# Optimization experiments

Measured on AMD Instinct MI355X. Metric: run time of the kernel, lower is better.

The kernel has to match this reference:

```python
import jax, jax.numpy as jnp
import numpy as np

N = 10000      # nodes (attention_adj_matrix_shape = (N, N))
E = 320000     # edges, avg degree 32
D_IN = 256     # input feature dim
D_H = 256      # hidden_units = [256]
ALPHA = 0.2    # leaky_relu slope for attention activation


def setup_inputs() -> dict:
    key = jax.random.key(0)
    k_x, k_src, k_dst, k_w1, k_b1, k_wa, k_ba = jax.random.split(key, 7)
    node_features = jax.random.normal(k_x, (N, D_IN), dtype=jnp.float32)
    # edges sorted by source column (tf.math.segment_sum requires sorted segment ids)
    src = jnp.sort(jax.random.randint(k_src, (E,), 0, N))
    dst = jax.random.randint(k_dst, (E,), 0, N)
    edges = jnp.stack([src, dst], axis=1).astype(jnp.int64)
    # hidden_layer: single Dense(256) (linear, keras Dense default activation=None)
    W1 = jax.random.normal(k_w1, (D_IN, D_H), dtype=jnp.float32) / np.sqrt(D_IN)
    b1 = jnp.zeros((D_H,), dtype=jnp.float32)
    # attention_layer: Dense(1) then activation
    Wa = jax.random.normal(k_wa, (2 * D_H, 1), dtype=jnp.float32) / np.sqrt(2 * D_H)
    ba = jnp.zeros((1,), dtype=jnp.float32)
    return {"node_features": node_features, "edges": edges,
            "W1": W1, "b1": b1, "Wa": Wa, "ba": ba}


def reference(node_features, edges, W1, b1, Wa, ba):
    n = node_features.shape[0]
    # hidden projection
    feats = node_features @ W1 + b1                       # [N, D_H]
    src, dst = edges[:, 0], edges[:, 1]
    # pairwise gather + concat: [E, 2*D_H]
    pair = jnp.concatenate([feats[src], feats[dst]], axis=1)
    scores = jax.nn.leaky_relu((pair @ Wa + ba)[:, 0], ALPHA)  # [E]
    # segment softmax over source node (matches exp / segment_sum / gather)
    ex = jnp.exp(scores)
    denom = jax.ops.segment_sum(ex, src, num_segments=n)       # [N]
    alpha = ex / denom[src]                                     # [E]
    # dense scatter of attention weights (scatter_nd sums duplicates)
    A = jnp.zeros((n, n), dtype=feats.dtype).at[src, dst].add(alpha)
    # add_self_features=False -> plain aggregate
    return A @ feats                                            # [N, D_H]
```

## Files before the change

kernel.cpp:

```cpp
#include <hip/hip_runtime.h>
#include <hip/hip_bf16.h>

#define N_NODES 10000
#define E_EDGES 320000
#define D 256
#define LRELU_ALPHA 0.2f


using short8  = __attribute__((ext_vector_type(8))) short;
using floatx4 = __attribute__((ext_vector_type(4))) float;
using bf16 = __hip_bfloat16;

__device__ __forceinline__ float bu2f(unsigned short u) {
    return __uint_as_float((unsigned)u << 16);
}
__device__ __forceinline__ unsigned short f2bu(float f) {
    union { bf16 b; unsigned short u; } cv;
    cv.b = __float2bfloat16(f);
    return cv.u;
}

__global__ __launch_bounds__(256) void prep(const int* __restrict__ raw,
                                            int* __restrict__ dst,
                                            int* __restrict__ row_start) {
    bool is64 = true;
    #pragma unroll
    for (int t = 0; t < 16; ++t)
        if (raw[2 * t + 1] != 0) is64 = false;

    int e = blockIdx.x * 256 + threadIdx.x;
    if (e >= E_EDGES) return;
    int s, d, sprev;
    if (is64) { s = raw[4 * e]; d = raw[4 * e + 2]; sprev = e ? raw[4 * e - 4] : -1; }
    else      { s = raw[2 * e]; d = raw[2 * e + 1]; sprev = e ? raw[2 * e - 2] : -1; }
    dst[e] = d;
    for (int r = sprev + 1; r <= s; ++r) row_start[r] = e;
    if (e == E_EDGES - 1)
        for (int r = s + 1; r <= N_NODES; ++r) row_start[r] = E_EDGES;
}

__global__ __launch_bounds__(256) void wprep(const float* __restrict__ W1,
                                             bf16* __restrict__ W1f) {
    const int id = blockIdx.x * 256 + threadIdx.x;
    const int j = id & 7, l = (id >> 3) & 63, t = (id >> 9) & 15, s = id >> 13;
    const int k = s * 32 + (l >> 4) * 8 + j;
    const int n = t * 16 + (l & 15);
    W1f[id] = __float2bfloat16(W1[k * D + n]);
}

__global__ __launch_bounds__(256) void gemm_mfma(const float* __restrict__ X,
                                                 const bf16* __restrict__ W1f,
                                                 const float* __restrict__ b1,
                                                 const float* __restrict__ Wa,
                                                 bf16* __restrict__ featsb,
                                                 float* __restrict__ a_src,
                                                 float* __restrict__ a_dst) {
    const int w = threadIdx.x >> 6, l = threadIdx.x & 63;
    const int quad = l >> 4, lan = l & 15;
    const int row0 = blockIdx.x * 16;

    floatx4 acc[4] = {{0.f, 0.f, 0.f, 0.f}, {0.f, 0.f, 0.f, 0.f},
                      {0.f, 0.f, 0.f, 0.f}, {0.f, 0.f, 0.f, 0.f}};

    const float4* Ax = (const float4*)(X + (size_t)(row0 + lan) * D);
    const short8* B8 = (const short8*)W1f;

    #pragma unroll
    for (int s = 0; s < 8; ++s) {
        const float4 u = Ax[s * 8 + quad * 2];
        const float4 v = Ax[s * 8 + quad * 2 + 1];
        short8 af;
        af[0] = (short)f2bu(u.x); af[1] = (short)f2bu(u.y);
        af[2] = (short)f2bu(u.z); af[3] = (short)f2bu(u.w);
        af[4] = (short)f2bu(v.x); af[5] = (short)f2bu(v.y);
        af[6] = (short)f2bu(v.z); af[7] = (short)f2bu(v.w);
        #pragma unroll
        for (int t = 0; t < 4; ++t) {
            const short8 bf = B8[(s * 16 + (4 * w + t)) * 64 + l];
            acc[t] = __builtin_amdgcn_mfma_f32_16x16x32_bf16(af, bf, acc[t], 0, 0, 0);
        }
    }

    float p1[4] = {0.f, 0.f, 0.f, 0.f}, p2[4] = {0.f, 0.f, 0.f, 0.f};
    #pragma unroll
    for (int t = 0; t < 4; ++t) {
        const int n = (4 * w + t) * 16 + lan;
        const float bias = b1[n], wa1 = Wa[n], wa2 = Wa[D + n];
        #pragma unroll
        for (int r = 0; r < 4; ++r) {
            const float v = acc[t][r] + bias;
            featsb[(size_t)(row0 + quad * 4 + r) * D + n] = __float2bfloat16(v);
            p1[r] += v * wa1;
            p2[r] += v * wa2;
        }
    }

    __shared__ float red1[4][16], red2[4][16];
    #pragma unroll
    for (int r = 0; r < 4; ++r) {
        #pragma unroll
        for (int off = 1; off < 16; off <<= 1) {
            p1[r] += __shfl_xor(p1[r], off);
            p2[r] += __shfl_xor(p2[r], off);
        }
        if (lan == 0) { red1[w][quad * 4 + r] = p1[r]; red2[w][quad * 4 + r] = p2[r]; }
    }
    __syncthreads();
    if (threadIdx.x < 16) {
        const int m = threadIdx.x;
        a_src[row0 + m] = red1[0][m] + red1[1][m] + red1[2][m] + red1[3][m];
        a_dst[row0 + m] = red2[0][m] + red2[1][m] + red2[2][m] + red2[3][m];
    }
}

__global__ __launch_bounds__(256) void aggregate_half(const int* __restrict__ dst,
                                                      const int* __restrict__ row_start,
                                                      const float* __restrict__ a_src,
                                                      const float* __restrict__ a_dst,
                                                      const float* __restrict__ ba,
                                                      const unsigned short* __restrict__ featsb,
                                                      float* __restrict__ out,
                                                      const int half) {
    const int i = blockIdx.x * 4 + (threadIdx.x >> 6);
    const int l = threadIdx.x & 63;
    const int rs = row_start[i], re = row_start[i + 1];
    const float base = a_src[i] + ba[0];
    const unsigned int* F = (const unsigned int*)featsb;
    const int off = half * 64 + l;

    float2 acc = {0.f, 0.f};
    float dsum = 0.f;

    int e = rs;
    for (; e + 8 <= re; e += 8) {
        unsigned int fw[8];
        float xv[8];
        #pragma unroll
        for (int u = 0; u < 8; ++u) {
            const int d = dst[e + u];
            fw[u] = F[(size_t)d * 128 + off];
            float s = base + a_dst[d];
            s = (s > 0.f) ? s : LRELU_ALPHA * s;
            xv[u] = expf(s);
        }
        #pragma unroll
        for (int u = 0; u < 8; ++u) {
            acc.x += xv[u] * bu2f((unsigned short)(fw[u] & 0xffff));
            acc.y += xv[u] * bu2f((unsigned short)(fw[u] >> 16));
            dsum += xv[u];
        }
    }
    for (; e < re; ++e) {
        const int d = dst[e];
        const unsigned int f = F[(size_t)d * 128 + off];
        float s = base + a_dst[d];
        s = (s > 0.f) ? s : LRELU_ALPHA * s;
        const float x = expf(s);
        acc.x += x * bu2f((unsigned short)(f & 0xffff));
        acc.y += x * bu2f((unsigned short)(f >> 16));
        dsum += x;
    }

    const float inv = (re > rs) ? 1.f / dsum : 0.f;
    float2 o;
    o.x = acc.x * inv;
    o.y = acc.y * inv;
    ((float2*)out)[(size_t)i * 128 + off] = o;
}

extern "C" void kernel_launch(void* const* d_in, const int* in_sizes, int n_in,
                              void* d_out, int out_size, void* d_ws, size_t ws_size,
                              hipStream_t stream) {
    const float* X     = (const float*)d_in[0];
    const int*   edges = (const int*)d_in[1];
    const float* W1    = (const float*)d_in[2];
    const float* b1    = (const float*)d_in[3];
    const float* Wa    = (const float*)d_in[4];
    const float* ba    = (const float*)d_in[5];
    float* out = (float*)d_out;

    bf16* featsb = (bf16*)d_ws;
    bf16* W1f    = featsb + (size_t)N_NODES * D;
    float* a_src = (float*)(W1f + 65536);
    float* a_dst = a_src + N_NODES;
    int*   dstv  = (int*)(a_dst + N_NODES);
    int*   row_start = dstv + E_EDGES;

    prep<<<(E_EDGES + 255) / 256, 256, 0, stream>>>(edges, dstv, row_start);
    wprep<<<65536 / 256, 256, 0, stream>>>(W1, W1f);
    gemm_mfma<<<N_NODES / 16, 256, 0, stream>>>(X, W1f, b1, Wa, featsb, a_src, a_dst);
    aggregate_half<<<N_NODES / 4, 256, 0, stream>>>(dstv, row_start, a_src, a_dst, ba,
                                                    (const unsigned short*)featsb, out, 0);
    aggregate_half<<<N_NODES / 4, 256, 0, stream>>>(dstv, row_start, a_src, a_dst, ba,
                                                    (const unsigned short*)featsb, out, 1);
}
```

Before: 123.0 us.

## Precompute per-edge attention weights in prep and merge aggregate halves into one pass

```diff
diff --git a/kernel.cpp b/kernel.cpp
--- a/kernel.cpp
+++ b/kernel.cpp
@@ -18,25 +18,6 @@
     union { bf16 b; unsigned short u; } cv;
     cv.b = __float2bfloat16(f);
     return cv.u;
-}
-
-__global__ __launch_bounds__(256) void prep(const int* __restrict__ raw,
-                                            int* __restrict__ dst,
-                                            int* __restrict__ row_start) {
-    bool is64 = true;
-    #pragma unroll
-    for (int t = 0; t < 16; ++t)
-        if (raw[2 * t + 1] != 0) is64 = false;
-
-    int e = blockIdx.x * 256 + threadIdx.x;
-    if (e >= E_EDGES) return;
-    int s, d, sprev;
-    if (is64) { s = raw[4 * e]; d = raw[4 * e + 2]; sprev = e ? raw[4 * e - 4] : -1; }
-    else      { s = raw[2 * e]; d = raw[2 * e + 1]; sprev = e ? raw[2 * e - 2] : -1; }
-    dst[e] = d;
-    for (int r = sprev + 1; r <= s; ++r) row_start[r] = e;
-    if (e == E_EDGES - 1)
-        for (int r = s + 1; r <= N_NODES; ++r) row_start[r] = E_EDGES;
 }
 
 __global__ __launch_bounds__(256) void wprep(const float* __restrict__ W1,
@@ -113,59 +94,71 @@
     }
 }
 
-__global__ __launch_bounds__(256) void aggregate_half(const int* __restrict__ dst,
-                                                      const int* __restrict__ row_start,
-                                                      const float* __restrict__ a_src,
-                                                      const float* __restrict__ a_dst,
-                                                      const float* __restrict__ ba,
-                                                      const unsigned short* __restrict__ featsb,
-                                                      float* __restrict__ out,
-                                                      const int half) {
+__global__ __launch_bounds__(256) void prep(const int* __restrict__ raw,
+                                            const float* __restrict__ a_src,
+                                            const float* __restrict__ a_dst,
+                                            const float* __restrict__ ba,
+                                            int2* __restrict__ edata,
+                                            int* __restrict__ row_start) {
+    bool is64 = true;
+    #pragma unroll
+    for (int t = 0; t < 16; ++t)
+        if (raw[2 * t + 1] != 0) is64 = false;
+
+    int e = blockIdx.x * 256 + threadIdx.x;
+    if (e >= E_EDGES) return;
+    int s, d, sprev;
+    if (is64) { s = raw[4 * e]; d = raw[4 * e + 2]; sprev = e ? raw[4 * e - 4] : -1; }
+    else      { s = raw[2 * e]; d = raw[2 * e + 1]; sprev = e ? raw[2 * e - 2] : -1; }
+
+    float sc = a_src[s] + a_dst[d] + ba[0];
+    sc = (sc > 0.f) ? sc : LRELU_ALPHA * sc;
+    edata[e] = make_int2(d, __float_as_int(expf(sc)));
+
+    for (int r = sprev + 1; r <= s; ++r) row_start[r] = e;
+    if (e == E_EDGES - 1)
+        for (int r = s + 1; r <= N_NODES; ++r) row_start[r] = E_EDGES;
+}
+
+__global__ __launch_bounds__(256) void aggregate(const int2* __restrict__ edata,
+                                                 const int* __restrict__ row_start,
+                                                 const unsigned short* __restrict__ featsb,
+                                                 float* __restrict__ out) {
     const int i = blockIdx.x * 4 + (threadIdx.x >> 6);
     const int l = threadIdx.x & 63;
     const int rs = row_start[i], re = row_start[i + 1];
-    const float base = a_src[i] + ba[0];
-    const unsigned int* F = (const unsigned int*)featsb;
-    const int off = half * 64 + l;
+    const ushort4* F = (const ushort4*)featsb;
 
-    float2 acc = {0.f, 0.f};
+    float4 acc = {0.f, 0.f, 0.f, 0.f};
     float dsum = 0.f;
 
     int e = rs;
     for (; e + 8 <= re; e += 8) {
-        unsigned int fw[8];
-        float xv[8];
+        int2 ed[8];
+        #pragma unroll
+        for (int u = 0; u < 8; ++u) ed[u] = edata[e + u];
         #pragma unroll
         for (int u = 0; u < 8; ++u) {
-            const int d = dst[e + u];
-            fw[u] = F[(size_t)d * 128 + off];
-            float s = base + a_dst[d];
-            s = (s > 0.f) ? s : LRELU_ALPHA * s;
-            xv[u] = expf(s);
-        }
-        #pragma unroll
-        for (int u = 0; u < 8; ++u) {
-            acc.x += xv[u] * bu2f((unsigned short)(fw[u] & 0xffff));
-            acc.y += xv[u] * bu2f((unsigned short)(fw[u] >> 16));
-            dsum += xv[u];
+            const ushort4 f = F[(size_t)ed[u].x * 64 + l];
+            const float x = __int_as_float(ed[u].y);
+            acc.x += x * bu2f(f.x); acc.y += x * bu2f(f.y);
+            acc.z += x * bu2f(f.z); acc.w += x * bu2f(f.w);
+            dsum += x;
         }
     }
     for (; e < re; ++e) {
-        const int d = dst[e];
-        const unsigned int f = F[(size_t)d * 128 + off];
-        float s = base + a_dst[d];
-        s = (s > 0.f) ? s : LRELU_ALPHA * s;
-        const float x = expf(s);
-        acc.x += x * bu2f((unsigned short)(f & 0xffff));
-        acc.y += x * bu2f((unsigned short)(f >> 16));
+        const int2 ed = edata[e];
+        const ushort4 f = F[(size_t)ed.x * 64 + l];
+        const float x = __int_as_float(ed.y);
+        acc.x += x * bu2f(f.x); acc.y += x * bu2f(f.y);
+        acc.z += x * bu2f(f.z); acc.w += x * bu2f(f.w);
         dsum += x;
     }
 
     const float inv = (re > rs) ? 1.f / dsum : 0.f;
-    float2 o;
-    o.x = acc.x * inv;
-    o.y = acc.y * inv;
-    ((float2*)out)[(size_t)i * 128 + off] = o;
+    float4 o;
+    o.x = acc.x * inv; o.y = acc.y * inv; o.z = acc.z * inv; o.w = acc.w * inv;
+    ((float4*)out)[(size_t)i * 64 + l] = o;
 }
 
 extern "C" void kernel_launch(void* const* d_in, const int* in_sizes, int n_in,
@@ -183,14 +176,12 @@
     bf16* W1f    = featsb + (size_t)N_NODES * D;
     float* a_src = (float*)(W1f + 65536);
     float* a_dst = a_src + N_NODES;
-    int*   dstv  = (int*)(a_dst + N_NODES);
-    int*   row_start = dstv + E_EDGES;
+    int2*  edata = (int2*)(a_dst + N_NODES);
+    int*   row_start = (int*)(edata + E_EDGES);
 
-    prep<<<(E_EDGES + 255) / 256, 256, 0, stream>>>(edges, dstv, row_start);
     wprep<<<65536 / 256, 256, 0, stream>>>(W1, W1f);
     gemm_mfma<<<N_NODES / 16, 256, 0, stream>>>(X, W1f, b1, Wa, featsb, a_src, a_dst);
-    aggregate_half<<<N_NODES / 4, 256, 0, stream>>>(dstv, row_start, a_src, a_dst, ba,
-                                                    (const unsigned short*)featsb, out, 0);
-    aggregate_half<<<N_NODES / 4, 256, 0, stream>>>(dstv, row_start, a_src, a_dst, ba,
-                                                    (const unsigned short*)featsb, out, 1);
+    prep<<<(E_EDGES + 255) / 256, 256, 0, stream>>>(edges, a_src, a_dst, ba, edata, row_start);
+    aggregate<<<N_NODES / 4, 256, 0, stream>>>(edata, row_start,
+                                               (const unsigned short*)featsb, out);
 }
```

Measured after the change: 108.7 us. 11.6% less time.
